# Optimization experiments

Hardware: AMD Instinct MI355X
Metric: run time of the kernel (lower is better)

Reference implementation:

```python
import jax, jax.numpy as jnp
import numpy as np

N, IN, OUT = 262144, 256, 256
EPS_MIN = 1e-10


def setup_inputs() -> dict:
    key = jax.random.key(0)
    k1, k2, k3 = jax.random.split(key, 3)
    x = jax.random.normal(k1, (N, IN), dtype=jnp.float32)
    weight = jax.random.normal(k2, (OUT, IN), dtype=jnp.float32) * 0.05
    bias = jax.random.normal(k3, (OUT,), dtype=jnp.float32) * 0.02
    return {"x": x, "weight": weight, "bias": bias}


def reference(x, weight, bias):
    # Mean-center weight rows and input rows (dim=1 in torch)
    wc = weight - jnp.mean(weight, axis=1, keepdims=True)          # [out, in]
    xc = x - jnp.mean(x, axis=1, keepdims=True)                    # [N, in]
    # temp_linear with all-ones weight == row-sum of xc^2, broadcast over out
    x_len = jax.lax.stop_gradient(
        jnp.sqrt(jnp.sum(xc * xc, axis=1, keepdims=True)))          # [N, 1]
    # temp_linear(ones_like(x)) with weight wc^2 == row-sum of wc^2 per out
    w_len = jax.lax.stop_gradient(
        jnp.sqrt(jnp.sum(wc * wc, axis=1)))                          # [out]
    # Correlation: centered GEMM, normalized, clamped; bias added after clamp
    corr = jnp.einsum('ni,oi->no', xc, wc) / (x_len * w_len[None, :])
    out = jnp.clip(corr, EPS_MIN, None) + bias[None, :]
    return out
```

## Files before the change

kernel.cpp:

```cpp
#include <hip/hip_runtime.h>
#include <hip/hip_bf16.h>


#define K_DIM 256
#define N_OUT 256
#define BM 64
#define LDS_STRIDE 264

typedef __attribute__((ext_vector_type(8))) __bf16 bf16x8;
typedef __attribute__((ext_vector_type(8))) unsigned short u16x8;
typedef __attribute__((ext_vector_type(4))) float f32x4;

__device__ __forceinline__ unsigned short f2bf(float f) {
    union { float f; unsigned u; } v; v.f = f;
    unsigned r = v.u + 0x7FFFu + ((v.u >> 16) & 1u);
    return (unsigned short)(r >> 16);
}

__global__ __launch_bounds__(64) void prep_w(const float* __restrict__ w,
                                             unsigned short* __restrict__ wcb) {
    int o = blockIdx.x;
    int lane = threadIdx.x;
    f32x4 v = *((const f32x4*)(w + (size_t)o * K_DIM) + lane);
    float s  = v.x + v.y + v.z + v.w;
    float s2 = v.x*v.x + v.y*v.y + v.z*v.z + v.w*v.w;
#pragma unroll
    for (int off = 32; off >= 1; off >>= 1) {
        s  += __shfl_xor(s,  off);
        s2 += __shfl_xor(s2, off);
    }
    float mean  = s * (1.0f / 256.0f);
    float var   = s2 - s * mean;
    float scale = rsqrtf(fmaxf(var, 1e-30f));
    ushort4 b;
    b.x = f2bf((v.x - mean) * scale);
    b.y = f2bf((v.y - mean) * scale);
    b.z = f2bf((v.z - mean) * scale);
    b.w = f2bf((v.w - mean) * scale);
    *(ushort4*)(wcb + (size_t)o * K_DIM + lane * 4) = b;
}

__global__ __launch_bounds__(256, 4) void pcc_gemm(const float* __restrict__ x,
                                                   const unsigned short* __restrict__ wcb,
                                                   const float* __restrict__ bias,
                                                   float* __restrict__ out) {
    __shared__ unsigned short xs[BM * LDS_STRIDE];
    __shared__ float nrm[BM];

    const int t    = threadIdx.x;
    const int wave = t >> 6;
    const int lane = t & 63;
    const int l15  = lane & 15;
    const int q    = lane >> 4;
    const size_t row0 = (size_t)blockIdx.x * BM;

    const int srow = wave * 16 + l15;
    const float* rp = x + (row0 + srow) * K_DIM + q * 64;

    f32x4 v[16];
#pragma unroll
    for (int j = 0; j < 16; ++j) v[j] = ((const f32x4*)rp)[j];

    const int n0 = wave * 64;
    float bv[4];
#pragma unroll
    for (int ni = 0; ni < 4; ++ni) bv[ni] = bias[n0 + ni * 16 + l15];

    unsigned short* wp = xs + srow * LDS_STRIDE + q * 64;
#pragma unroll
    for (int j = 0; j < 8; ++j) {
        u16x8 p;
        p[0] = f2bf(v[2*j].x);   p[1] = f2bf(v[2*j].y);
        p[2] = f2bf(v[2*j].z);   p[3] = f2bf(v[2*j].w);
        p[4] = f2bf(v[2*j+1].x); p[5] = f2bf(v[2*j+1].y);
        p[6] = f2bf(v[2*j+1].z); p[7] = f2bf(v[2*j+1].w);
        *(u16x8*)(wp + j * 8) = p;
    }

    float s = 0.f, s2 = 0.f;
#pragma unroll
    for (int j = 0; j < 16; ++j) {
        s += v[j].x + v[j].y + v[j].z + v[j].w;
        s2 = fmaf(v[j].x, v[j].x, s2);
        s2 = fmaf(v[j].y, v[j].y, s2);
        s2 = fmaf(v[j].z, v[j].z, s2);
        s2 = fmaf(v[j].w, v[j].w, s2);
    }
    s  += __shfl_xor(s, 16);  s  += __shfl_xor(s, 32);
    s2 += __shfl_xor(s2, 16); s2 += __shfl_xor(s2, 32);
    float var = s2 - s * s * (1.0f / 256.0f);
    float inv = rsqrtf(fmaxf(var, 1e-30f));
    if (q == 0) nrm[srow] = inv;
    __syncthreads();

    f32x4 acc[4][4];
#pragma unroll
    for (int mi = 0; mi < 4; ++mi)
#pragma unroll
        for (int ni = 0; ni < 4; ++ni)
            acc[mi][ni] = (f32x4){0.f, 0.f, 0.f, 0.f};

    const unsigned short* wbase = wcb + (size_t)n0 * K_DIM + q * 8;

#pragma unroll
    for (int ks = 0; ks < 8; ++ks) {
        bf16x8 a[4], b[4];
#pragma unroll
        for (int mi = 0; mi < 4; ++mi)
            a[mi] = *(const bf16x8*)(xs + (mi * 16 + l15) * LDS_STRIDE + ks * 32 + q * 8);
#pragma unroll
        for (int ni = 0; ni < 4; ++ni)
            b[ni] = *(const bf16x8*)(wbase + (size_t)(ni * 16 + l15) * K_DIM + ks * 32);
#pragma unroll
        for (int mi = 0; mi < 4; ++mi)
#pragma unroll
            for (int ni = 0; ni < 4; ++ni)
                acc[mi][ni] = __builtin_amdgcn_mfma_f32_16x16x32_bf16(a[mi], b[ni], acc[mi][ni], 0, 0, 0);
    }

    float invv[4][4];
#pragma unroll
    for (int mi = 0; mi < 4; ++mi)
#pragma unroll
        for (int r = 0; r < 4; ++r)
            invv[mi][r] = nrm[mi * 16 + q * 4 + r];

    float* obase = out + row0 * N_OUT;
#pragma unroll
    for (int mi = 0; mi < 4; ++mi) {
#pragma unroll
        for (int r = 0; r < 4; ++r) {
            const int orow = mi * 16 + q * 4 + r;
            float* op = obase + (size_t)orow * N_OUT + n0 + l15;
#pragma unroll
            for (int ni = 0; ni < 4; ++ni)
                op[ni * 16] = fmaxf(acc[mi][ni][r] * invv[mi][r], 1e-10f) + bv[ni];
        }
    }
}

extern "C" void kernel_launch(void* const* d_in, const int* in_sizes, int n_in,
                              void* d_out, int out_size, void* d_ws, size_t ws_size,
                              hipStream_t stream) {
    const float* x    = (const float*)d_in[0];
    const float* w    = (const float*)d_in[1];
    const float* bias = (const float*)d_in[2];
    float* out = (float*)d_out;
    unsigned short* wcb = (unsigned short*)d_ws;

    prep_w<<<256, 64, 0, stream>>>(w, wcb);
    pcc_gemm<<<262144 / BM, 256, 0, stream>>>(x, wcb, bias, out);
}
```

Before: 474.5 us.

## Persistent GEMM with async global-to-LDS double buffering and register-resident weights

```diff
diff --git a/kernel.cpp b/kernel.cpp
--- a/kernel.cpp
+++ b/kernel.cpp
@@ -4,12 +4,16 @@
 
 #define K_DIM 256
 #define N_OUT 256
-#define BM 64
-#define LDS_STRIDE 264
+#define BM    64
+#define ROW_F 260
+#define TILES 8
+#define NBLK  512
 
 typedef __attribute__((ext_vector_type(8))) __bf16 bf16x8;
-typedef __attribute__((ext_vector_type(8))) unsigned short u16x8;
-typedef __attribute__((ext_vector_type(4))) float f32x4;
+typedef __attribute__((ext_vector_type(4))) float  f32x4;
+
+typedef const __attribute__((address_space(1))) unsigned int* gp1_t;
+typedef __attribute__((address_space(3))) unsigned int*       lp3_t;
 
 __device__ __forceinline__ unsigned short f2bf(float f) {
     union { float f; unsigned u; } v; v.f = f;
@@ -40,101 +44,123 @@
     *(ushort4*)(wcb + (size_t)o * K_DIM + lane * 4) = b;
 }
 
-__global__ __launch_bounds__(256, 4) void pcc_gemm(const float* __restrict__ x,
+__global__ __launch_bounds__(512, 2) void pcc_gemm(const float* __restrict__ x,
                                                    const unsigned short* __restrict__ wcb,
                                                    const float* __restrict__ bias,
                                                    float* __restrict__ out) {
-    __shared__ unsigned short xs[BM * LDS_STRIDE];
+    __shared__ __align__(16) float sb[2][BM * ROW_F];
     __shared__ float nrm[BM];
 
     const int t    = threadIdx.x;
-    const int wave = t >> 6;
+    const int w    = t >> 6;
     const int lane = t & 63;
     const int l15  = lane & 15;
     const int q    = lane >> 4;
-    const size_t row0 = (size_t)blockIdx.x * BM;
+    const int wr   = w >> 2;
+    const int wc   = w & 3;
 
-    const int srow = wave * 16 + l15;
-    const float* rp = x + (row0 + srow) * K_DIM + q * 64;
-
-    f32x4 v[16];
-#pragma unroll
-    for (int j = 0; j < 16; ++j) v[j] = ((const f32x4*)rp)[j];
-
-    const int n0 = wave * 64;
-    float bv[4];
-#pragma unroll
-    for (int ni = 0; ni < 4; ++ni) bv[ni] = bias[n0 + ni * 16 + l15];
-
-    unsigned short* wp = xs + srow * LDS_STRIDE + q * 64;
-#pragma unroll
-    for (int j = 0; j < 8; ++j) {
-        u16x8 p;
-        p[0] = f2bf(v[2*j].x);   p[1] = f2bf(v[2*j].y);
-        p[2] = f2bf(v[2*j].z);   p[3] = f2bf(v[2*j].w);
-        p[4] = f2bf(v[2*j+1].x); p[5] = f2bf(v[2*j+1].y);
-        p[6] = f2bf(v[2*j+1].z); p[7] = f2bf(v[2*j+1].w);
-        *(u16x8*)(wp + j * 8) = p;
-    }
-
-    float s = 0.f, s2 = 0.f;
-#pragma unroll
-    for (int j = 0; j < 16; ++j) {
-        s += v[j].x + v[j].y + v[j].z + v[j].w;
-        s2 = fmaf(v[j].x, v[j].x, s2);
-        s2 = fmaf(v[j].y, v[j].y, s2);
-        s2 = fmaf(v[j].z, v[j].z, s2);
-        s2 = fmaf(v[j].w, v[j].w, s2);
-    }
-    s  += __shfl_xor(s, 16);  s  += __shfl_xor(s, 32);
-    s2 += __shfl_xor(s2, 16); s2 += __shfl_xor(s2, 32);
-    float var = s2 - s * s * (1.0f / 256.0f);
-    float inv = rsqrtf(fmaxf(var, 1e-30f));
-    if (q == 0) nrm[srow] = inv;
-    __syncthreads();
-
-    f32x4 acc[4][4];
-#pragma unroll
-    for (int mi = 0; mi < 4; ++mi)
+    bf16x8 bfrag[8][4];
+    {
+        const unsigned short* wb = wcb + (size_t)(wc * 64 + l15) * K_DIM + q * 8;
 #pragma unroll
         for (int ni = 0; ni < 4; ++ni)
-            acc[mi][ni] = (f32x4){0.f, 0.f, 0.f, 0.f};
+#pragma unroll
+            for (int ks = 0; ks < 8; ++ks)
+                bfrag[ks][ni] = *(const bf16x8*)(wb + (size_t)(ni * 16) * K_DIM + ks * 32);
+    }
+    f32x4 bb[4];
+#pragma unroll
+    for (int ni = 0; ni < 4; ++ni)
+        bb[ni] = *(const f32x4*)(bias + wc * 64 + ni * 16 + q * 4);
 
-    const unsigned short* wbase = wcb + (size_t)n0 * K_DIM + q * 8;
+    const size_t tile0 = (size_t)blockIdx.x * TILES;
+    const int myrow = w * 8 + (lane >> 3);
+    const int seg   = lane & 7;
 
+    auto issue = [&](int tt, int bufi) {
+        const float* src = x + ((tile0 + tt) * BM + w * 8) * (size_t)K_DIM + lane * 4;
+        float* dst = &sb[bufi][(w * 8) * ROW_F];
 #pragma unroll
-    for (int ks = 0; ks < 8; ++ks) {
-        bf16x8 a[4], b[4];
+        for (int r = 0; r < 8; ++r)
+            __builtin_amdgcn_global_load_lds((gp1_t)(src + (size_t)r * K_DIM),
+                                             (lp3_t)(dst + r * ROW_F), 16, 0, 0);
+    };
+
+    issue(0, 0);
+
+    for (int tt = 0; tt < TILES; ++tt) {
+        const int cur = tt & 1;
+
+        if (tt == 0) { asm volatile("s_waitcnt vmcnt(0)" ::: "memory"); }
+        else         { asm volatile("s_waitcnt vmcnt(8)" ::: "memory"); }
+        __builtin_amdgcn_sched_barrier(0);
+        __builtin_amdgcn_s_barrier();
+        __builtin_amdgcn_sched_barrier(0);
+
+        if (tt + 1 < TILES) issue(tt + 1, cur ^ 1);
+
+        {
+            const float* rp = &sb[cur][myrow * ROW_F + seg * 32];
+            float s = 0.f, s2 = 0.f;
 #pragma unroll
-        for (int mi = 0; mi < 4; ++mi)
-            a[mi] = *(const bf16x8*)(xs + (mi * 16 + l15) * LDS_STRIDE + ks * 32 + q * 8);
+            for (int j = 0; j < 8; ++j) {
+                f32x4 v = *(const f32x4*)(rp + j * 4);
+                s += v.x + v.y + v.z + v.w;
+                s2 = fmaf(v.x, v.x, s2); s2 = fmaf(v.y, v.y, s2);
+                s2 = fmaf(v.z, v.z, s2); s2 = fmaf(v.w, v.w, s2);
+            }
+            s  += __shfl_xor(s, 1);  s  += __shfl_xor(s, 2);  s  += __shfl_xor(s, 4);
+            s2 += __shfl_xor(s2, 1); s2 += __shfl_xor(s2, 2); s2 += __shfl_xor(s2, 4);
+            if (seg == 0) {
+                float var = s2 - s * s * (1.0f / 256.0f);
+                nrm[myrow] = rsqrtf(fmaxf(var, 1e-30f));
+            }
+        }
+        asm volatile("s_waitcnt lgkmcnt(0)" ::: "memory");
+        __builtin_amdgcn_sched_barrier(0);
+        __builtin_amdgcn_s_barrier();
+        __builtin_amdgcn_sched_barrier(0);
+
+        f32x4 acc[2][4];
 #pragma unroll
-        for (int ni = 0; ni < 4; ++ni)
-            b[ni] = *(const bf16x8*)(wbase + (size_t)(ni * 16 + l15) * K_DIM + ks * 32);
-#pragma unroll
-        for (int mi = 0; mi < 4; ++mi)
+        for (int mi = 0; mi < 2; ++mi)
 #pragma unroll
             for (int ni = 0; ni < 4; ++ni)
-                acc[mi][ni] = __builtin_amdgcn_mfma_f32_16x16x32_bf16(a[mi], b[ni], acc[mi][ni], 0, 0, 0);
-    }
+                acc[mi][ni] = (f32x4){0.f, 0.f, 0.f, 0.f};
 
-    float invv[4][4];
+        const float* ab = &sb[cur][(wr * 32 + l15) * ROW_F + q * 8];
 #pragma unroll
-    for (int mi = 0; mi < 4; ++mi)
+        for (int ks = 0; ks < 8; ++ks) {
 #pragma unroll
-        for (int r = 0; r < 4; ++r)
-            invv[mi][r] = nrm[mi * 16 + q * 4 + r];
+            for (int mi = 0; mi < 2; ++mi) {
+                const float* ap = ab + mi * 16 * ROW_F + ks * 32;
+                f32x4 lo = *(const f32x4*)ap;
+                f32x4 hi = *(const f32x4*)(ap + 4);
+                bf16x8 a;
+                a[0] = (__bf16)lo.x; a[1] = (__bf16)lo.y;
+                a[2] = (__bf16)lo.z; a[3] = (__bf16)lo.w;
+                a[4] = (__bf16)hi.x; a[5] = (__bf16)hi.y;
+                a[6] = (__bf16)hi.z; a[7] = (__bf16)hi.w;
+#pragma unroll
+                for (int ni = 0; ni < 4; ++ni)
+                    acc[mi][ni] = __builtin_amdgcn_mfma_f32_16x16x32_bf16(
+                        bfrag[ks][ni], a, acc[mi][ni], 0, 0, 0);
+            }
+        }
 
-    float* obase = out + row0 * N_OUT;
+        const size_t grow = (tile0 + tt) * BM + wr * 32 + l15;
 #pragma unroll
-    for (int mi = 0; mi < 4; ++mi) {
+        for (int mi = 0; mi < 2; ++mi) {
+            const float inv = nrm[wr * 32 + mi * 16 + l15];
+            float* op = out + (grow + (size_t)mi * 16) * N_OUT + wc * 64 + q * 4;
 #pragma unroll
-        for (int r = 0; r < 4; ++r) {
-            const int orow = mi * 16 + q * 4 + r;
-            float* op = obase + (size_t)orow * N_OUT + n0 + l15;
+            for (int ni = 0; ni < 4; ++ni) {
+                f32x4 vx;
 #pragma unroll
-            for (int ni = 0; ni < 4; ++ni)
-                op[ni * 16] = fmaxf(acc[mi][ni][r] * invv[mi][r], 1e-10f) + bv[ni];
+                for (int r = 0; r < 4; ++r)
+                    vx[r] = fmaxf(acc[mi][ni][r] * inv, 1e-10f) + bb[ni][r];
+                __builtin_nontemporal_store(vx, (f32x4*)(op + ni * 16));
+            }
         }
     }
 }
@@ -149,5 +175,5 @@
     unsigned short* wcb = (unsigned short*)d_ws;
 
     prep_w<<<256, 64, 0, stream>>>(w, wcb);
-    pcc_gemm<<<262144 / BM, 256, 0, stream>>>(x, wcb, bias, out);
+    pcc_gemm<<<NBLK, 512, 0, stream>>>(x, wcb, bias, out);
 }
```

Measured after the change: 493.8 us. +4.1%, slower.
